# Kernel optimization log

Measured on AMD Instinct MI355X. Metric: run time of the kernel, lower is better.

Reference implementation:

```python
import jax, jax.numpy as jnp
import numpy as np

N = 500000   # total nodes
D = 128      # feature dim
S = 2048     # number of graphs (segments)
BETA = 1.0
EPS = 1e-16  # matches torch_geometric.utils.softmax denominator epsilon


def setup_inputs() -> dict:
    key = jax.random.key(0)
    k1, k2 = jax.random.split(key)
    x = jax.random.normal(k1, (N, D), dtype=jnp.float32)
    batch = jnp.sort(jax.random.randint(k2, (N,), 0, S, dtype=jnp.int64))
    return {"x": x, "batch": batch, "size": S}


def reference(x, batch, size):
    # per-segment (per-graph) softmax over nodes, per feature channel
    z = BETA * x                                   # [N, D]
    m = jax.ops.segment_max(z, batch, num_segments=size)  # [S, D]
    m = jnp.where(jnp.isfinite(m), m, jnp.zeros_like(m))  # empty segments -> 0
    ex = jnp.exp(z - m[batch])                     # [N, D]
    denom = jax.ops.segment_sum(ex, batch, num_segments=size)  # [S, D]
    soft = ex / (denom[batch] + EPS)               # [N, D]
    # scatter-mean of x * softmax weights
    weighted_sum = jax.ops.segment_sum(x * soft, batch, num_segments=size)  # [S, D]
    cnt = jax.ops.segment_sum(jnp.ones((x.shape[0], 1), x.dtype), batch, num_segments=size)  # [S, 1]
    out = weighted_sum / jnp.maximum(cnt, 1.0)
    return out
```

## Files before the change

### kernel.cpp

```cpp
#include <hip/hip_runtime.h>
#include <math.h>

#define DCH 128
#define NV  (DCH / 4)
#define RG  8
#define BLK (NV * RG)
#define LOG2E 1.44269504088896340736f

typedef float f32x4 __attribute__((ext_vector_type(4)));

__global__ __launch_bounds__(BLK) void seg_softmax_pool_kernel(
    const float* __restrict__ x, const void* __restrict__ batch,
    int N, int S, float* __restrict__ out) {
    const int s   = blockIdx.x;
    const int tid = threadIdx.x;

    __shared__ int sb[2];
    if (tid == 0 || tid == 64) {
        const int* b32 = (const int*)batch;
        const bool is32 = (b32[N - 1] != 0);
        const int target = s + (tid >> 6);
        int lo = 0, hi = N;
        if (is32) {
            while (lo < hi) {
                int mid = (lo + hi) >> 1;
                if (b32[mid] < target) lo = mid + 1; else hi = mid;
            }
        } else {
            const long long* b64 = (const long long*)batch;
            const long long t = (long long)target;
            while (lo < hi) {
                int mid = (lo + hi) >> 1;
                if (b64[mid] < t) lo = mid + 1; else hi = mid;
            }
        }
        sb[tid >> 6] = lo;
    }
    __syncthreads();

    const int start = sb[0];
    const int end   = sb[1];
    const int cnt   = end - start;
    const int c4    = tid & (NV - 1);
    const int rg    = tid >> 5;

    if (cnt == 0) {
        if (tid < NV) {
            ((float4*)out)[s * NV + tid] = make_float4(0.f, 0.f, 0.f, 0.f);
        }
        return;
    }

    float4 se  = make_float4(0.f, 0.f, 0.f, 0.f);
    float4 sxe = make_float4(0.f, 0.f, 0.f, 0.f);

    const f32x4* __restrict__ xv = (const f32x4*)x;
    for (int n = start + rg; n < end; n += RG) {
        f32x4 v = __builtin_nontemporal_load(&xv[(size_t)n * NV + c4]);
        float ex = __builtin_amdgcn_exp2f(v.x * LOG2E);
        float ey = __builtin_amdgcn_exp2f(v.y * LOG2E);
        float ez = __builtin_amdgcn_exp2f(v.z * LOG2E);
        float ew = __builtin_amdgcn_exp2f(v.w * LOG2E);
        se.x += ex; sxe.x = fmaf(v.x, ex, sxe.x);
        se.y += ey; sxe.y = fmaf(v.y, ey, sxe.y);
        se.z += ez; sxe.z = fmaf(v.z, ez, sxe.z);
        se.w += ew; sxe.w = fmaf(v.w, ew, sxe.w);
    }

    __shared__ float4 smS[BLK], smX[BLK];
    smS[tid] = se; smX[tid] = sxe;
    __syncthreads();

    if (tid < NV) {
        float4 bs = smS[tid], bx = smX[tid];
        #pragma unroll
        for (int g = 1; g < RG; ++g) {
            float4 s2 = smS[g * NV + tid];
            float4 x2 = smX[g * NV + tid];
            bs.x += s2.x; bs.y += s2.y; bs.z += s2.z; bs.w += s2.w;
            bx.x += x2.x; bx.y += x2.y; bx.z += x2.z; bx.w += x2.w;
        }
        const float inv_cnt = 1.0f / (float)cnt;
        float4 o;
        o.x = bx.x / (bs.x + 1e-16f) * inv_cnt;
        o.y = bx.y / (bs.y + 1e-16f) * inv_cnt;
        o.z = bx.z / (bs.z + 1e-16f) * inv_cnt;
        o.w = bx.w / (bs.w + 1e-16f) * inv_cnt;
        ((float4*)out)[s * NV + tid] = o;
    }
}

extern "C" void kernel_launch(void* const* d_in, const int* in_sizes, int n_in,
                              void* d_out, int out_size, void* d_ws, size_t ws_size,
                              hipStream_t stream) {
    const float* x    = (const float*)d_in[0];
    const void* batch = d_in[1];
    const int N = in_sizes[1];
    const int S = out_size / DCH;

    seg_softmax_pool_kernel<<<S, BLK, 0, stream>>>(x, batch, N, S,
                                                   (float*)d_out);
}
```

Baseline: 48.32 us.

## Split nodes into equal chunks with atomic per-segment partials and finalize pass

Replaces the one-block-per-segment design with a fixed grid of 2048 blocks that each take an equal contiguous chunk of nodes. Each block walks the segment runs inside its chunk, reduces exp and x*exp sums, and atomically adds them into workspace buffers; a second kernel then normalizes by the count. The aim is to balance load across blocks regardless of segment size and to drop the per-block binary searches. In exchange it adds a memset, a second launch, float atomics whose summation order is not fixed, and one extra block barrier per segment run. The shared batch buffer holds 256 entries, which assumes chunks of at most 256 nodes, true for N=500000.

```diff
diff --git a/kernel.cpp b/kernel.cpp
--- a/kernel.cpp
+++ b/kernel.cpp
@@ -5,16 +5,103 @@
 #define NV  (DCH / 4)
 #define RG  8
 #define BLK (NV * RG)
+#define G   2048
 #define LOG2E 1.44269504088896340736f
 
 typedef float f32x4 __attribute__((ext_vector_type(4)));
+
+__global__ __launch_bounds__(BLK) void seg_partial_kernel(
+    const float* __restrict__ x, const void* __restrict__ batch,
+    int N, float* __restrict__ ws_se, float* __restrict__ ws_sxe,
+    int* __restrict__ ws_cnt) {
+    const int b    = blockIdx.x;
+    const int base = N / G, rem = N % G;
+    const int c0   = b * base + min(b, rem);
+    const int csz  = base + (b < rem ? 1 : 0);
+    const int c1   = c0 + csz;
+    const int tid  = threadIdx.x;
+    const int c4   = tid & (NV - 1);
+    const int rg   = tid >> 5;
+
+    __shared__ int sbatch[256];
+    const int* b32 = (const int*)batch;
+    const bool is32 = (b32[N - 1] != 0);
+    if (is32) {
+        for (int i = tid; i < csz; i += BLK) sbatch[i] = b32[c0 + i];
+    } else {
+        const long long* b64 = (const long long*)batch;
+        for (int i = tid; i < csz; i += BLK) sbatch[i] = (int)b64[c0 + i];
+    }
+    __syncthreads();
+
+    __shared__ float4 smS[BLK], smX[BLK];
+    const f32x4* __restrict__ xv = (const f32x4*)x;
+
+    int p = c0;
+    while (p < c1) {
+        const int seg = sbatch[p - c0];
+        int q = p + 1;
+        while (q < c1 && sbatch[q - c0] == seg) ++q;
+
+        float4 se  = make_float4(0.f, 0.f, 0.f, 0.f);
+        float4 sxe = make_float4(0.f, 0.f, 0.f, 0.f);
+        for (int n = p + rg; n < q; n += RG) {
+            f32x4 v = __builtin_nontemporal_load(&xv[(size_t)n * NV + c4]);
+            float ex = __builtin_amdgcn_exp2f(v.x * LOG2E);
+            float ey = __builtin_amdgcn_exp2f(v.y * LOG2E);
+            float ez = __builtin_amdgcn_exp2f(v.z * LOG2E);
+            float ew = __builtin_amdgcn_exp2f(v.w * LOG2E);
+            se.x += ex; sxe.x = fmaf(v.x, ex, sxe.x);
+            se.y += ey; sxe.y = fmaf(v.y, ey, sxe.y);
+            se.z += ez; sxe.z = fmaf(v.z, ez, sxe.z);
+            se.w += ew; sxe.w = fmaf(v.w, ew, sxe.w);
+        }
+        smS[tid] = se; smX[tid] = sxe;
+        __syncthreads();
+        if (tid < NV) {
+            float4 bs = smS[tid], bx = smX[tid];
+            #pragma unroll
+            for (int g = 1; g < RG; ++g) {
+                float4 s2 = smS[g * NV + tid];
+                float4 x2 = smX[g * NV + tid];
+                bs.x += s2.x; bs.y += s2.y; bs.z += s2.z; bs.w += s2.w;
+                bx.x += x2.x; bx.y += x2.y; bx.z += x2.z; bx.w += x2.w;
+            }
+            float* pse = ws_se  + (size_t)seg * DCH + tid * 4;
+            float* psx = ws_sxe + (size_t)seg * DCH + tid * 4;
+            atomicAdd(pse + 0, bs.x); atomicAdd(pse + 1, bs.y);
+            atomicAdd(pse + 2, bs.z); atomicAdd(pse + 3, bs.w);
+            atomicAdd(psx + 0, bx.x); atomicAdd(psx + 1, bx.y);
+            atomicAdd(psx + 2, bx.z); atomicAdd(psx + 3, bx.w);
+        }
+        if (tid == 0) atomicAdd(&ws_cnt[seg], q - p);
+        __syncthreads();
+        p = q;
+    }
+}
+
+__global__ __launch_bounds__(BLK) void finalize_kernel(
+    const float* __restrict__ ws_se, const float* __restrict__ ws_sxe,
+    const int* __restrict__ ws_cnt, float* __restrict__ out, int SNV) {
+    const int gid = blockIdx.x * BLK + threadIdx.x;
+    if (gid >= SNV) return;
+    const int s = gid >> 5;
+    float4 se = ((const float4*)ws_se)[gid];
+    float4 sx = ((const float4*)ws_sxe)[gid];
+    const float inv = 1.0f / fmaxf((float)ws_cnt[s], 1.0f);
+    float4 o;
+    o.x = sx.x / (se.x + 1e-16f) * inv;
+    o.y = sx.y / (se.y + 1e-16f) * inv;
+    o.z = sx.z / (se.z + 1e-16f) * inv;
+    o.w = sx.w / (se.w + 1e-16f) * inv;
+    ((float4*)out)[gid] = o;
+}
 
 __global__ __launch_bounds__(BLK) void seg_softmax_pool_kernel(
     const float* __restrict__ x, const void* __restrict__ batch,
     int N, int S, float* __restrict__ out) {
     const int s   = blockIdx.x;
     const int tid = threadIdx.x;
-
     __shared__ int sb[2];
     if (tid == 0 || tid == 64) {
         const int* b32 = (const int*)batch;
@@ -22,38 +109,24 @@
         const int target = s + (tid >> 6);
         int lo = 0, hi = N;
         if (is32) {
-            while (lo < hi) {
-                int mid = (lo + hi) >> 1;
-                if (b32[mid] < target) lo = mid + 1; else hi = mid;
-            }
+            while (lo < hi) { int mid = (lo + hi) >> 1;
+                if (b32[mid] < target) lo = mid + 1; else hi = mid; }
         } else {
             const long long* b64 = (const long long*)batch;
             const long long t = (long long)target;
-            while (lo < hi) {
-                int mid = (lo + hi) >> 1;
-                if (b64[mid] < t) lo = mid + 1; else hi = mid;
-            }
+            while (lo < hi) { int mid = (lo + hi) >> 1;
+                if (b64[mid] < t) lo = mid + 1; else hi = mid; }
         }
         sb[tid >> 6] = lo;
     }
     __syncthreads();
-
-    const int start = sb[0];
-    const int end   = sb[1];
-    const int cnt   = end - start;
-    const int c4    = tid & (NV - 1);
-    const int rg    = tid >> 5;
-
+    const int start = sb[0], end = sb[1], cnt = end - start;
+    const int c4 = tid & (NV - 1), rg = tid >> 5;
     if (cnt == 0) {
-        if (tid < NV) {
-            ((float4*)out)[s * NV + tid] = make_float4(0.f, 0.f, 0.f, 0.f);
-        }
+        if (tid < NV) ((float4*)out)[s * NV + tid] = make_float4(0,0,0,0);
         return;
     }
-
-    float4 se  = make_float4(0.f, 0.f, 0.f, 0.f);
-    float4 sxe = make_float4(0.f, 0.f, 0.f, 0.f);
-
+    float4 se  = make_float4(0,0,0,0), sxe = make_float4(0,0,0,0);
     const f32x4* __restrict__ xv = (const f32x4*)x;
     for (int n = start + rg; n < end; n += RG) {
         f32x4 v = __builtin_nontemporal_load(&xv[(size_t)n * NV + c4]);
@@ -66,17 +139,14 @@
         se.z += ez; sxe.z = fmaf(v.z, ez, sxe.z);
         se.w += ew; sxe.w = fmaf(v.w, ew, sxe.w);
     }
-
     __shared__ float4 smS[BLK], smX[BLK];
     smS[tid] = se; smX[tid] = sxe;
     __syncthreads();
-
     if (tid < NV) {
         float4 bs = smS[tid], bx = smX[tid];
         #pragma unroll
         for (int g = 1; g < RG; ++g) {
-            float4 s2 = smS[g * NV + tid];
-            float4 x2 = smX[g * NV + tid];
+            float4 s2 = smS[g * NV + tid], x2 = smX[g * NV + tid];
             bs.x += s2.x; bs.y += s2.y; bs.z += s2.z; bs.w += s2.w;
             bx.x += x2.x; bx.y += x2.y; bx.z += x2.z; bx.w += x2.w;
         }
@@ -98,6 +168,21 @@
     const int N = in_sizes[1];
     const int S = out_size / DCH;
 
-    seg_softmax_pool_kernel<<<S, BLK, 0, stream>>>(x, batch, N, S,
-                                                   (float*)d_out);
+    const size_t se_bytes  = (size_t)S * DCH * sizeof(float);
+    const size_t need      = 2 * se_bytes + (size_t)S * sizeof(int);
+
+    if (ws_size >= need) {
+        float* ws_se  = (float*)d_ws;
+        float* ws_sxe = (float*)((char*)d_ws + se_bytes);
+        int*   ws_cnt = (int*)((char*)d_ws + 2 * se_bytes);
+        hipMemsetAsync(d_ws, 0, need, stream);
+        seg_partial_kernel<<<G, BLK, 0, stream>>>(x, batch, N,
+                                                  ws_se, ws_sxe, ws_cnt);
+        const int SNV = S * NV;
+        finalize_kernel<<<(SNV + BLK - 1) / BLK, BLK, 0, stream>>>(
+            ws_se, ws_sxe, ws_cnt, (float*)d_out, SNV);
+    } else {
+        seg_softmax_pool_kernel<<<S, BLK, 0, stream>>>(x, batch, N, S,
+                                                       (float*)d_out);
+    }
 }
```

Result: slower. 77.79 us (+61.0%).
